# Performance work log

Measured on AMD Instinct MI355X. Metric: run time of the kernel, lower is better.

The kernel has to match this reference:

```python
import jax, jax.numpy as jnp
import numpy as np

D_IN = 1024
D_OUT = 1024

def setup_inputs() -> dict:
    key = jax.random.key(0)
    kx, kq, kk, kv = jax.random.split(key, 4)
    X = jax.random.normal(kx, (4, 2048, D_IN), dtype=jnp.float32)
    s = 1.0 / np.sqrt(D_IN)
    Wq = jax.random.uniform(kq, (D_IN, D_OUT), jnp.float32, -s, s)
    Wk = jax.random.uniform(kk, (D_IN, D_OUT), jnp.float32, -s, s)
    Wv = jax.random.uniform(kv, (D_IN, D_OUT), jnp.float32, -s, s)
    return {"X": X, "Wq": Wq, "Wk": Wk, "Wv": Wv}

def reference(X, Wq, Wk, Wv):
    # X: [b, s, d_in]; W*: [d_in, d_out] (torch Linear weight transposed)
    B, S, _ = X.shape
    q = jnp.einsum('bsd,de->bse', X, Wq)
    k = jnp.einsum('bsd,de->bse', X, Wk)
    v = jnp.einsum('bsd,de->bse', X, Wv)
    scores = jnp.einsum('bqe,bke->bqk', q, k)  # [b, s, s]
    causal = jnp.triu(jnp.ones((S, S), dtype=bool), k=1)
    scores = jnp.where(causal, -jnp.inf, scores)
    weights = jax.nn.softmax(scores / jnp.sqrt(jnp.asarray(k.shape[-1], scores.dtype)), axis=-1)
    # dropout p=0.0 (eval) -> identity
    return jnp.einsum('bqk,bke->bqe', weights, v)
```

## Files before the change

### kernel.cpp

```cpp
#include <hip/hip_runtime.h>
#include <cstdint>
#include <cmath>

typedef unsigned short u16;
typedef u16   u16x4  __attribute__((ext_vector_type(4)));
typedef u16   u16x8  __attribute__((ext_vector_type(8)));
typedef __bf16 bf16x8 __attribute__((ext_vector_type(8)));
typedef float f32x4  __attribute__((ext_vector_type(4)));

__device__ __forceinline__ u16 f2bf(float f) {
    uint32_t u = __builtin_bit_cast(uint32_t, f);
    u += 0x7fffu + ((u >> 16) & 1u);
    return (u16)(u >> 16);
}
__device__ __forceinline__ float bf2f(u16 v) {
    uint32_t u = ((uint32_t)v) << 16;
    return __builtin_bit_cast(float, u);
}
__device__ __forceinline__ void gload_lds16(const u16* g, u16* l) {
    __builtin_amdgcn_global_load_lds((const __attribute__((address_space(1))) void*)g,
                                     (__attribute__((address_space(3))) void*)l,
                                     16, 0, 0);
}

__global__ __launch_bounds__(256) void prep_kernel(const float* __restrict__ X,
                                                   const float* __restrict__ Wq,
                                                   const float* __restrict__ Wk,
                                                   const float* __restrict__ Wv,
                                                   u16* __restrict__ Xb,
                                                   u16* __restrict__ Wt) {
    __shared__ u16 tile[64 * 72];
    typedef float f4 __attribute__((ext_vector_type(4)));
    const int bid = blockIdx.x;
    if (bid < 8192) {
        const int idx = bid * 256 + threadIdx.x;
        f4 f = ((const f4*)X)[idx];
        u16x4 o;
        o[0] = f2bf(f[0]); o[1] = f2bf(f[1]); o[2] = f2bf(f[2]); o[3] = f2bf(f[3]);
        ((u16x4*)Xb)[idx] = o;
        return;
    }
    const int id = bid - 8192;
    const int z = id >> 8, rem = id & 255;
    const float* W = (z == 0) ? Wq : (z == 1) ? Wk : Wv;
    u16* out = Wt + ((size_t)z << 20);
    const int nt = (rem & 15) * 64, kt = (rem >> 4) * 64;
    const int t = threadIdx.x, r = t >> 2, cq = (t & 3) * 16;
    const float* src = W + (size_t)(kt + r) * 1024 + nt + cq;
#pragma unroll
    for (int q = 0; q < 4; q++) {
        f4 f = ((const f4*)src)[q];
        tile[r * 72 + cq + q * 4 + 0] = f2bf(f[0]);
        tile[r * 72 + cq + q * 4 + 1] = f2bf(f[1]);
        tile[r * 72 + cq + q * 4 + 2] = f2bf(f[2]);
        tile[r * 72 + cq + q * 4 + 3] = f2bf(f[3]);
    }
    __syncthreads();
    u16x8 o0, o1;
#pragma unroll
    for (int e = 0; e < 8; e++) { o0[e] = tile[(cq + e) * 72 + r]; o1[e] = tile[(cq + 8 + e) * 72 + r]; }
    u16* dst = out + (size_t)(nt + r) * 1024 + kt + cq;
    *(u16x8*)dst = o0;
    *(u16x8*)(dst + 8) = o1;
}

template <int OUTMODE>
__device__ __forceinline__ void gemm_bt_core(u16* __restrict__ smem,
                                             const u16* __restrict__ A,
                                             const u16* __restrict__ Bt,
                                             void* __restrict__ outp,
                                             const int ldk, const int ldo,
                                             const int kbeg, const int kend,
                                             const int m0, const int n0,
                                             const int om0, const int on0) {
    u16* As = smem;
    u16* Bs = smem + 4096;
    const int tid = (int)threadIdx.x;
    const int wave = tid >> 6, lane = tid & 63;
    const int wm = wave >> 1, wn = wave & 1;

    f32x4 acc[4][4] = {};

    const int sr = lane >> 2;
    const int scw = ((lane & 3) ^ ((sr >> 1) & 3)) * 8;
    const u16* gA = A  + (size_t)(m0 + wave * 32 + sr) * ldk + scw;
    const u16* gB = Bt + (size_t)(n0 + wave * 32 + sr) * ldk + scw;
    u16* lA = As + wave * 1024;
    u16* lB = Bs + wave * 1024;
    const size_t rstep = (size_t)ldk * 16;

    const int arow = lane & 15;
    const int ksw  = (arow >> 1) & 3;
    const int koff = (((lane >> 4) ^ ksw)) * 8;
    const u16* pa = As + (wm * 64 + arow) * 32 + koff;
    const u16* pb = Bs + (wn * 64 + arow) * 32 + koff;

    for (int k0 = kbeg; k0 < kend; k0 += 32) {
        gload_lds16(gA + k0,         lA);
        gload_lds16(gA + k0 + rstep, lA + 512);
        gload_lds16(gB + k0,         lB);
        gload_lds16(gB + k0 + rstep, lB + 512);
        __syncthreads();
        bf16x8 a[4], b[4];
#pragma unroll
        for (int i = 0; i < 4; i++) a[i] = *(const bf16x8*)(pa + i * 512);
#pragma unroll
        for (int j = 0; j < 4; j++) b[j] = *(const bf16x8*)(pb + j * 512);
#pragma unroll
        for (int i = 0; i < 4; i++)
#pragma unroll
            for (int j = 0; j < 4; j++)
                acc[i][j] = __builtin_amdgcn_mfma_f32_16x16x32_bf16(a[i], b[j], acc[i][j], 0, 0, 0);
        __syncthreads();
    }

    const int row0 = om0 + wm * 64 + ((lane >> 4) << 2);
    const int col0 = on0 + wn * 64 + (lane & 15);
    if constexpr (OUTMODE == 0) {
        u16* o = (u16*)outp;
#pragma unroll
        for (int i = 0; i < 4; i++)
#pragma unroll
            for (int r = 0; r < 4; r++) {
                u16* po = o + (size_t)(row0 + i * 16 + r) * ldo + col0;
#pragma unroll
                for (int j = 0; j < 4; j++) po[j * 16] = f2bf(acc[i][j][r]);
            }
    } else {
        float* o = (float*)outp;
#pragma unroll
        for (int i = 0; i < 4; i++)
#pragma unroll
            for (int r = 0; r < 4; r++) {
                float* po = o + (size_t)(row0 + i * 16 + r) * ldo + col0;
#pragma unroll
                for (int j = 0; j < 4; j++) po[j * 16] = acc[i][j][r];
            }
    }
}

__global__ __launch_bounds__(512, 2) void qkv_gemm_kernel(const u16* __restrict__ Xb,
                                                          const u16* __restrict__ Wt,
                                                          u16* __restrict__ QKV) {
    __shared__ u16 lds[49152];
    const int bid = blockIdx.x;
    const int xcd = bid & 7, slot = bid >> 3;
    const int z = slot >> 5, r32 = slot & 31;
    const int m0 = (xcd * 4 + (r32 >> 3)) << 8;
    const int n0 = (r32 & 7) << 7;

    const u16* __restrict__ A = Xb;
    const u16* __restrict__ B = Wt + ((size_t)z << 20);
    u16* __restrict__ C = QKV + ((size_t)z << 23);

    const int tid = (int)threadIdx.x;
    const int w = tid >> 6, l = tid & 63;
    const int wm = w >> 2, wn = w & 3;

    const int srow = w * 16 + (l >> 3);
    const int scol = ((l & 7) ^ ((l >> 3) & 7)) * 8;
    const u16* gA = A + (size_t)(m0 + srow) * 1024 + scol;
    const u16* gB = B + (size_t)(n0 + srow) * 1024 + scol;
    u16* const sA = lds + w * 1024;
    u16* const sB = lds + 32768 + w * 1024;

    const int c0 = ((l >> 4) ^ (l & 7)) * 8;
    const u16* const pa_ = lds + (wm * 64 + (l & 15)) * 64;
    const u16* const pb_ = lds + 32768 + (wn * 32 + (l & 15)) * 64;

    f32x4 acc[2][4][2] = {};
    bf16x8 a[4][2], b[2][2];

#define MFMA_ __builtin_amdgcn_mfma_f32_16x16x32_bf16
#define STG_A(BUF, H, T) \
    gload_lds16(gA + (size_t)((H) * 128) * 1024 + (T) * 64,       sA + (BUF) + (H) * 8192); \
    gload_lds16(gA + (size_t)((H) * 128 + 8) * 1024 + (T) * 64,   sA + (BUF) + (H) * 8192 + 512);
#define STG_B(BUF, T) \
    gload_lds16(gB + (T) * 64,                                    sB + ((BUF) >> 1)); \
    gload_lds16(gB + (size_t)8 * 1024 + (T) * 64,                 sB + ((BUF) >> 1) + 512);
#define LD_A(BUF, QA) \
    _Pragma("unroll") for (int m_ = 0; m_ < 4; m_++) { \
        a[m_][0] = *(const bf16x8*)(pa_ + (BUF) + (QA) * 8192 + m_ * 1024 + c0); \
        a[m_][1] = *(const bf16x8*)(pa_ + (BUF) + (QA) * 8192 + m_ * 1024 + (c0 ^ 32)); \
    }
#define LD_B(BUF) \
    _Pragma("unroll") for (int n_ = 0; n_ < 2; n_++) { \
        b[n_][0] = *(const bf16x8*)(pb_ + ((BUF) >> 1) + n_ * 1024 + c0); \
        b[n_][1] = *(const bf16x8*)(pb_ + ((BUF) >> 1) + n_ * 1024 + (c0 ^ 32)); \
    }
#define MM(QA) \
    _Pragma("unroll") for (int m_ = 0; m_ < 4; m_++) { \
        _Pragma("unroll") for (int n_ = 0; n_ < 2; n_++) { \
            acc[QA][m_][n_] = MFMA_(a[m_][0], b[n_][0], acc[QA][m_][n_], 0, 0, 0); \
            acc[QA][m_][n_] = MFMA_(a[m_][1], b[n_][1], acc[QA][m_][n_], 0, 0, 0); \
        } \
    }
#define VM6 asm volatile("s_waitcnt vmcnt(6)" ::: "memory");
#define VM2 asm volatile("s_waitcnt vmcnt(2)" ::: "memory");
#define VM0 asm volatile("s_waitcnt vmcnt(0)" ::: "memory");
#define VMN
#define BAR __builtin_amdgcn_s_barrier();
#define PRIO1 __builtin_amdgcn_s_setprio(1);
#define PRIO0 __builtin_amdgcn_s_setprio(0);
#define TILE(BUF, OBUF, T1, S1, T2, S2, VMA, VMB) \
    LD_A(BUF, 0) LD_B(BUF) \
    if (S1) { STG_A(OBUF, 1, T1) } \
    VMA BAR PRIO1 MM(0) PRIO0 BAR \
    LD_A(BUF, 1) \
    if (S2) { STG_A(BUF, 0, T2) STG_B(BUF, T2) } \
    VMB BAR PRIO1 MM(1) PRIO0 BAR

    STG_A(0, 0, 0) STG_B(0, 0) STG_A(0, 1, 0)
    STG_A(16384, 0, 1) STG_B(16384, 1)
    asm volatile("s_waitcnt vmcnt(6)" ::: "memory");
    __builtin_amdgcn_s_barrier();

#pragma unroll 1
    for (int i = 0; i < 7; ++i) {
        const int t1 = 2 * i + 1, t2 = 2 * i + 2, t3 = 2 * i + 3;
        TILE(0,     16384, t1, 1, t2, 1, VM6, VM6)
        TILE(16384, 0,     t2, 1, t3, 1, VM6, VM6)
    }
    TILE(0,     16384, 15, 1, 0, 0, VM6, VM2)
    TILE(16384, 0,     0,  0, 0, 0, VM0, VMN)

    const int row0 = m0 + wm * 64 + ((l >> 4) << 2);
    const int col0 = n0 + wn * 32 + (l & 15);
#pragma unroll
    for (int qa = 0; qa < 2; qa++)
#pragma unroll
        for (int m = 0; m < 4; m++)
#pragma unroll
            for (int r = 0; r < 4; r++) {
                u16* po = C + (size_t)(row0 + qa * 128 + m * 16 + r) * 1024 + col0;
#pragma unroll
                for (int n = 0; n < 2; n++) po[n * 16] = f2bf(acc[qa][m][n][r]);
            }
#undef MFMA_
#undef STG_A
#undef STG_B
#undef LD_A
#undef LD_B
#undef MM
#undef VM6
#undef VM2
#undef VM0
#undef VMN
#undef BAR
#undef PRIO1
#undef PRIO0
#undef TILE
}

__global__ __launch_bounds__(256) void s_tr_kernel(const u16* __restrict__ QKV,
                                                   u16* __restrict__ S,
                                                   u16* __restrict__ Vt) {
    __shared__ u16 smem[8192];
    const int bid = blockIdx.x;
    if (bid < 576) {
        const int xcd = bid & 7, slot = bid >> 3;
        const int b = xcd >> 1, half = xcd & 1;
        int it = half ? 11 : 0;
        const int ntiles = half ? 70 : 66;
        if (slot >= ntiles) return;
        int acc = 0;
        while (acc + it + 1 <= slot) { acc += it + 1; it++; }
        const int jt = slot - acc;
        const u16* Q  = QKV + ((size_t)b << 21);
        const u16* Kp = QKV + ((size_t)1 << 23) + ((size_t)b << 21);
        gemm_bt_core<0>(smem, Q, Kp, S + ((size_t)b << 22), 1024, 2048, 0, 1024,
                        it * 128, jt * 128, it * 128, jt * 128);
        return;
    }
    const int id = bid - 576;
    const int z = id >> 9, rem = id & 511;
    const u16* src = QKV + ((size_t)2 << 23) + ((size_t)z << 21);
    u16* dst = Vt + ((size_t)z << 21);
    const int st = (rem & 31) * 64, et = (rem >> 5) * 64;
    u16 (*tile)[72] = (u16(*)[72])smem;
    const int t = threadIdx.x, r = t >> 2, cq = (t & 3) * 16;
    const u16* p = src + (size_t)(st + r) * 1024 + et + cq;
    u16x8 u0 = *(const u16x8*)p;
    u16x8 u1 = *(const u16x8*)(p + 8);
#pragma unroll
    for (int e = 0; e < 8; e++) { tile[r][cq + e] = u0[e]; tile[r][cq + 8 + e] = u1[e]; }
    __syncthreads();
    u16x8 o0, o1;
#pragma unroll
    for (int e = 0; e < 8; e++) { o0[e] = tile[cq + e][r]; o1[e] = tile[cq + 8 + e][r]; }
    u16* q = dst + (size_t)(et + r) * 2048 + st + cq;
    *(u16x8*)q = o0;
    *(u16x8*)(q + 8) = o1;
}

__global__ __launch_bounds__(256) void pv_gemm_kernel(const u16* __restrict__ P,
                                                      const u16* __restrict__ Vt,
                                                      float* __restrict__ O) {
    __shared__ u16 smem[8192];
    const int j = blockIdx.x;
    const int phase = j >> 8, c = j & 255;
    const int slot = c >> 5, combo = c & 31;
    const int it = phase ? (15 - slot) : slot;
    const int b = combo >> 3, n0 = (combo & 7) * 128;
    gemm_bt_core<1>(smem, P + ((size_t)b << 22), Vt + ((size_t)b << 21),
                    O + ((size_t)b << 21),
                    2048, 1024, 0, (it + 1) * 128, it * 128, n0, it * 128, n0);
}

__global__ __launch_bounds__(256) void softmax_kernel(u16* __restrict__ S) {
    const int wave = threadIdx.x >> 6, lane = threadIdx.x & 63;
    const int g = blockIdx.x * 4 + wave;
    const int b = g >> 11, i = g & 2047;
    u16* row = S + ((size_t)b << 22) + ((size_t)i << 11);
    const int n = i + 1;
    const int kend = ((i >> 7) + 1) << 7;
    const int nt_ = (kend + 511) >> 9;
    const float NEG = -1e30f;
    float v[32];
    float m = NEG;
#pragma unroll
    for (int t = 0; t < 4; t++) {
        if (t < nt_) {
            u16x8 u = *(const u16x8*)(row + t * 512 + lane * 8);
#pragma unroll
            for (int e = 0; e < 8; e++) {
                const int col = t * 512 + lane * 8 + e;
                float f = (col < n) ? bf2f(u[e]) : NEG;
                v[t * 8 + e] = f;
                m = fmaxf(m, f);
            }
        }
    }
#pragma unroll
    for (int off = 32; off > 0; off >>= 1) m = fmaxf(m, __shfl_xor(m, off, 64));
    const float sc = 0.03125f * 1.44269504088896f;
    float s = 0.f;
#pragma unroll
    for (int t = 0; t < 4; t++) {
        if (t < nt_) {
#pragma unroll
            for (int e = 0; e < 8; e++) {
                const float x = v[t * 8 + e];
                const float e2 = (x == NEG) ? 0.f : exp2f((x - m) * sc);
                v[t * 8 + e] = e2;
                s += e2;
            }
        }
    }
#pragma unroll
    for (int off = 32; off > 0; off >>= 1) s += __shfl_xor(s, off, 64);
    const float inv = 1.f / s;
#pragma unroll
    for (int t = 0; t < 4; t++) {
        if (t < nt_) {
            u16x8 o;
#pragma unroll
            for (int e = 0; e < 8; e++) o[e] = f2bf(v[t * 8 + e] * inv);
            *(u16x8*)(row + t * 512 + lane * 8) = o;
        }
    }
}

extern "C" void kernel_launch(void* const* d_in, const int* in_sizes, int n_in,
                              void* d_out, int out_size, void* d_ws, size_t ws_size,
                              hipStream_t stream) {
    const float* X  = (const float*)d_in[0];
    const float* Wq = (const float*)d_in[1];
    const float* Wk = (const float*)d_in[2];
    const float* Wv = (const float*)d_in[3];
    float* out = (float*)d_out;

    u16* ws  = (u16*)d_ws;
    u16* Xb  = ws;
    u16* Wt  = Xb + ((size_t)1 << 23);
    u16* QKV = Wt + 3 * ((size_t)1 << 20);
    u16* S   = QKV + 3 * ((size_t)1 << 23);
    u16* Vt  = Xb;

    prep_kernel<<<8960, 256, 0, stream>>>(X, Wq, Wk, Wv, Xb, Wt);
    qkv_gemm_kernel<<<768, 512, 0, stream>>>(Xb, Wt, QKV);
    s_tr_kernel<<<2624, 256, 0, stream>>>(QKV, S, Vt);
    softmax_kernel<<<2048, 256, 0, stream>>>(S);
    pv_gemm_kernel<<<512, 256, 0, stream>>>(S, Vt, out);
}
```

Before: 239.3 us.

## Rewrite PV GEMM with triple-buffered async LDS pipeline and paired causal tiles

Replaces the generic PV GEMM with a dedicated 512-thread kernel. Each block processes two 128-row tiles paired so their causal work sums to a constant (15-pair and pair), which balances load across blocks. K-steps are streamed through a triple-buffered LDS ring with direct global-to-LDS loads, XOR-swizzled layout, and vmcnt waits so loads overlap MFMA. Blocks are mapped to XCDs for L2 locality. The trade-off is higher LDS use and more barriers per step, and the launch halves to 256 blocks.

```diff
diff --git a/kernel.cpp b/kernel.cpp
--- a/kernel.cpp
+++ b/kernel.cpp
@@ -293,18 +293,102 @@
     *(u16x8*)(q + 8) = o1;
 }
 
-__global__ __launch_bounds__(256) void pv_gemm_kernel(const u16* __restrict__ P,
-                                                      const u16* __restrict__ Vt,
-                                                      float* __restrict__ O) {
-    __shared__ u16 smem[8192];
-    const int j = blockIdx.x;
-    const int phase = j >> 8, c = j & 255;
-    const int slot = c >> 5, combo = c & 31;
-    const int it = phase ? (15 - slot) : slot;
-    const int b = combo >> 3, n0 = (combo & 7) * 128;
-    gemm_bt_core<1>(smem, P + ((size_t)b << 22), Vt + ((size_t)b << 21),
-                    O + ((size_t)b << 21),
-                    2048, 1024, 0, (it + 1) * 128, it * 128, n0, it * 128, n0);
+__device__ __forceinline__ void pv_tile128(const u16* __restrict__ Pb,
+                                           const u16* __restrict__ Vb,
+                                           float* __restrict__ Ob,
+                                           u16* __restrict__ lds,
+                                           const int it, const int n0) {
+    const int tid = (int)threadIdx.x;
+    const int w = tid >> 6, l = tid & 63;
+    const int wm = w >> 2, wn = w & 3;
+    const int nk = 2 * (it + 1);
+    const int m0 = it * 128;
+
+    const int srow = w * 16 + (l >> 3);
+    const int scol = ((l & 7) ^ ((l >> 3) & 7)) * 8;
+    const u16* gA = Pb + (size_t)(m0 + srow) * 2048 + scol;
+    const u16* gB = Vb + (size_t)(n0 + srow) * 2048 + scol;
+    u16* const sA = lds + w * 1024;
+    u16* const sB = lds + 24576 + w * 1024;
+
+    const int c0 = ((l >> 4) ^ (l & 7)) * 8;
+    const u16* const pa_ = lds + (wm * 64 + (l & 15)) * 64;
+    const u16* const pb_ = lds + 24576 + (wn * 32 + (l & 15)) * 64;
+
+    f32x4 acc[4][2] = {};
+
+#define PSTG(T, BUF) \
+    gload_lds16(gA + (size_t)(T) * 64,                    sA + (BUF) * 8192); \
+    gload_lds16(gA + (size_t)(T) * 64 + (size_t)8 * 2048, sA + (BUF) * 8192 + 512); \
+    gload_lds16(gB + (size_t)(T) * 64,                    sB + (BUF) * 8192); \
+    gload_lds16(gB + (size_t)(T) * 64 + (size_t)8 * 2048, sB + (BUF) * 8192 + 512);
+
+    PSTG(0, 0) PSTG(1, 1)
+    asm volatile("s_waitcnt vmcnt(4)" ::: "memory");
+    __builtin_amdgcn_s_barrier();
+
+    int bufR = 0, bufW = 2;
+#pragma unroll 1
+    for (int t = 0; t < nk; ++t) {
+        bf16x8 a[4][2], b[2][2];
+#pragma unroll
+        for (int m = 0; m < 4; m++) {
+            a[m][0] = *(const bf16x8*)(pa_ + bufR * 8192 + m * 1024 + c0);
+            a[m][1] = *(const bf16x8*)(pa_ + bufR * 8192 + m * 1024 + (c0 ^ 32));
+        }
+#pragma unroll
+        for (int n = 0; n < 2; n++) {
+            b[n][0] = *(const bf16x8*)(pb_ + bufR * 8192 + n * 1024 + c0);
+            b[n][1] = *(const bf16x8*)(pb_ + bufR * 8192 + n * 1024 + (c0 ^ 32));
+        }
+        if (t < nk - 2) {
+            PSTG(t + 2, bufW)
+            asm volatile("s_waitcnt vmcnt(4)" ::: "memory");
+        } else {
+            asm volatile("s_waitcnt vmcnt(0)" ::: "memory");
+        }
+        __builtin_amdgcn_s_barrier();
+        __builtin_amdgcn_s_setprio(1);
+#pragma unroll
+        for (int m = 0; m < 4; m++)
+#pragma unroll
+            for (int n = 0; n < 2; n++) {
+                acc[m][n] = __builtin_amdgcn_mfma_f32_16x16x32_bf16(a[m][0], b[n][0], acc[m][n], 0, 0, 0);
+                acc[m][n] = __builtin_amdgcn_mfma_f32_16x16x32_bf16(a[m][1], b[n][1], acc[m][n], 0, 0, 0);
+            }
+        __builtin_amdgcn_s_setprio(0);
+        __builtin_amdgcn_s_barrier();
+        bufR = (bufR == 2) ? 0 : bufR + 1;
+        bufW = (bufW == 2) ? 0 : bufW + 1;
+    }
+#undef PSTG
+
+    const int row0 = m0 + wm * 64 + ((l >> 4) << 2);
+    const int col0 = n0 + wn * 32 + (l & 15);
+#pragma unroll
+    for (int m = 0; m < 4; m++)
+#pragma unroll
+        for (int r = 0; r < 4; r++) {
+            float* po = Ob + (size_t)(row0 + m * 16 + r) * 1024 + col0;
+#pragma unroll
+            for (int n = 0; n < 2; n++) po[n * 16] = acc[m][n][r];
+        }
+}
+
+__global__ __launch_bounds__(512, 2) void pv_gemm_kernel(const u16* __restrict__ P,
+                                                         const u16* __restrict__ Vt,
+                                                         float* __restrict__ O) {
+    __shared__ u16 lds[49152];
+    const int bid = blockIdx.x;
+    const int xcd = bid & 7, slot = bid >> 3;
+    const int combo = xcd * 4 + (slot >> 3);
+    const int n0 = (slot & 7) * 128;
+    const int pair = combo >> 2, b = combo & 3;
+    const u16* Pb = P + ((size_t)b << 22);
+    const u16* Vb = Vt + ((size_t)b << 21);
+    float* Ob = O + ((size_t)b << 21);
+    pv_tile128(Pb, Vb, Ob, lds, 15 - pair, n0);
+    pv_tile128(Pb, Vb, Ob, lds, pair, n0);
 }
 
 __global__ __launch_bounds__(256) void softmax_kernel(u16* __restrict__ S) {
@@ -381,5 +465,5 @@
     qkv_gemm_kernel<<<768, 512, 0, stream>>>(Xb, Wt, QKV);
     s_tr_kernel<<<2624, 256, 0, stream>>>(QKV, S, Vt);
     softmax_kernel<<<2048, 256, 0, stream>>>(S);
-    pv_gemm_kernel<<<512, 256, 0, stream>>>(S, Vt, out);
-}
+    pv_gemm_kernel<<<256, 512, 0, stream>>>(S, Vt, out);
+}
```

Measured after the change: 219.0 us. 8.5% less time.
